# Optimization experiments

Measured on AMD Instinct MI355X. Metric: run time of the kernel, lower is better.

The kernel has to match this reference:

```python
import jax, jax.numpy as jnp
import numpy as np

B, T, C = 2, 4096, 768
H = 12
D = C // H  # head_dim = 64

def setup_inputs() -> dict:
    key = jax.random.key(0)
    ks = jax.random.split(key, 5)
    s = 1.0 / np.sqrt(C)
    return {
        "x": jax.random.normal(ks[0], (B, T, C), dtype=jnp.float32),
        "qkv_w": jax.random.normal(ks[1], (C, 3 * C), dtype=jnp.float32) * s,
        "qkv_b": jax.random.normal(ks[2], (3 * C,), dtype=jnp.float32) * 0.02,
        "out_w": jax.random.normal(ks[3], (C, C), dtype=jnp.float32) * s,
        "out_b": jax.random.normal(ks[4], (C,), dtype=jnp.float32) * 0.02,
    }

def reference(x, qkv_w, qkv_b, out_w, out_b):
    b, t, c = x.shape
    qkv = x @ qkv_w + qkv_b                      # [B,T,3C]
    q, k, v = jnp.split(qkv, 3, axis=-1)
    # [B,T,C] -> [B,H,T,D]
    q = q.reshape(b, t, H, D).transpose(0, 2, 1, 3)
    k = k.reshape(b, t, H, D).transpose(0, 2, 1, 3)
    v = v.reshape(b, t, H, D).transpose(0, 2, 1, 3)
    scale = 1.0 / np.sqrt(D)
    attn = jnp.einsum('bhqd,bhkd->bhqk', q, k) * scale  # [B,H,T,T]
    causal = jnp.tril(jnp.ones((t, t), dtype=bool))
    attn = jnp.where(causal, attn, -jnp.inf)
    attn = jax.nn.softmax(attn, axis=-1)
    y = jnp.einsum('bhqk,bhkd->bhqd', attn, v)           # [B,H,T,D]
    y = y.transpose(0, 2, 1, 3).reshape(b, t, c)
    return y @ out_w + out_b
```

## Files before the change

### kernel.cpp

```cpp
#include <hip/hip_runtime.h>
#include <hip/hip_bf16.h>

#define T_SEQ 4096
#define C_DIM 768
#define H_NUM 12
#define D_HEAD 64
#define N3    2304
#define BHN   24

typedef __bf16 bf16x8 __attribute__((ext_vector_type(8)));
typedef float  f32x4  __attribute__((ext_vector_type(4)));

__device__ inline unsigned short f2b(float f) {
    unsigned int x = __float_as_uint(f);
    unsigned int r = (x + 0x7FFFu + ((x >> 16) & 1u)) >> 16;
    return (unsigned short)r;
}

__device__ inline unsigned int pack_trunc(float lo, float hi) {
    return __builtin_amdgcn_perm(__float_as_uint(hi), __float_as_uint(lo), 0x07060302u);
}

__device__ inline void load_lds16(const unsigned short* g, unsigned short* l) {
    __builtin_amdgcn_global_load_lds(
        (const __attribute__((address_space(1))) unsigned int*)(g),
        (__attribute__((address_space(3))) unsigned int*)(l),
        16, 0, 0);
}

__global__ __launch_bounds__(256) void convert_bf16(
    const float* __restrict__ in, unsigned short* __restrict__ out, int n4)
{
    int idx = blockIdx.x * 256 + threadIdx.x;
    if (idx < n4) {
        float4 v = reinterpret_cast<const float4*>(in)[idx];
        ushort4 u;
        u.x = f2b(v.x); u.y = f2b(v.y); u.z = f2b(v.z); u.w = f2b(v.w);
        reinterpret_cast<ushort4*>(out)[idx] = u;
    }
}

__global__ __launch_bounds__(256) void transpose_bf16(
    const float* __restrict__ in, unsigned short* __restrict__ out, int R, int Cc)
{
    __shared__ unsigned short Ts[64 * 72];
    const int k0 = blockIdx.x * 64, n0 = blockIdx.y * 64;
    const int tid = threadIdx.x;
    #pragma unroll
    for (int it = 0; it < 4; ++it) {
        int idx = tid + it * 256;
        int r = idx >> 4, c4 = idx & 15;
        float4 v = *reinterpret_cast<const float4*>(&in[(size_t)(k0 + r) * Cc + n0 + c4 * 4]);
        Ts[(c4 * 4 + 0) * 72 + r] = f2b(v.x);
        Ts[(c4 * 4 + 1) * 72 + r] = f2b(v.y);
        Ts[(c4 * 4 + 2) * 72 + r] = f2b(v.z);
        Ts[(c4 * 4 + 3) * 72 + r] = f2b(v.w);
    }
    __syncthreads();
    #pragma unroll
    for (int it = 0; it < 2; ++it) {
        int idx = tid + it * 256;
        int row = idx >> 3, ch = idx & 7;
        *reinterpret_cast<uint4*>(&out[(size_t)(n0 + row) * R + k0 + ch * 8]) =
            *reinterpret_cast<const uint4*>(&Ts[row * 72 + ch * 8]);
    }
}

__global__ __launch_bounds__(256) void qkv_gemm(
    const unsigned short* __restrict__ xb, const unsigned short* __restrict__ wt,
    const float* __restrict__ bias,
    unsigned short* __restrict__ Q, unsigned short* __restrict__ K,
    unsigned short* __restrict__ Vt)
{
    __shared__ unsigned short SH[128 * 128];
    unsigned short* As = SH;
    unsigned short* Bs = SH + 128 * 64;
    const int tid  = threadIdx.x;
    const int m0   = blockIdx.x * 128;
    const int n0   = blockIdx.y * 128;
    const int lane = tid & 63;
    const int wv   = tid >> 6;
    const int wr   = wv >> 1, wc = wv & 1;
    const int quad = lane >> 4;
    const int lr   = lane & 15;
    const int srow = lane >> 3;
    const int dch  = (lane & 7) ^ srow;

    f32x4 acc[4][4] = {};

    for (int kk = 0; kk < C_DIM; kk += 64) {
        __syncthreads();
        #pragma unroll
        for (int i = 0; i < 4; ++i) {
            int inst = wv * 4 + i;
            int r = inst * 8 + srow;
            load_lds16(xb + (size_t)(m0 + r) * C_DIM + kk + dch * 8, As + inst * 512);
            load_lds16(wt + (size_t)(n0 + r) * C_DIM + kk + dch * 8, Bs + inst * 512);
        }
        __syncthreads();
        #pragma unroll
        for (int k2 = 0; k2 < 2; ++k2) {
            bf16x8 af[4], bf[4];
            #pragma unroll
            for (int mt = 0; mt < 4; ++mt)
                af[mt] = *reinterpret_cast<const bf16x8*>(
                    &As[(wr * 64 + mt * 16 + lr) * 64 + (((k2 * 4 + quad) ^ (lr & 7)) * 8)]);
            #pragma unroll
            for (int nt = 0; nt < 4; ++nt)
                bf[nt] = *reinterpret_cast<const bf16x8*>(
                    &Bs[(wc * 64 + nt * 16 + lr) * 64 + (((k2 * 4 + quad) ^ (lr & 7)) * 8)]);
            #pragma unroll
            for (int mt = 0; mt < 4; ++mt)
                #pragma unroll
                for (int nt = 0; nt < 4; ++nt)
                    acc[mt][nt] = __builtin_amdgcn_mfma_f32_16x16x32_bf16(af[mt], bf[nt], acc[mt][nt], 0, 0, 0);
        }
    }

    const int whichblk = n0 / C_DIM;
    if (whichblk == 2) {
        __syncthreads();
        #pragma unroll
        for (int nt = 0; nt < 4; ++nt) {
            int dp = wc * 64 + nt * 16 + lr;
            float bj = bias[n0 + dp];
            #pragma unroll
            for (int mt = 0; mt < 4; ++mt) {
                int t0 = wr * 64 + mt * 16 + quad * 4;
                ushort4 u;
                u.x = f2b(acc[mt][nt][0] + bj);
                u.y = f2b(acc[mt][nt][1] + bj);
                u.z = f2b(acc[mt][nt][2] + bj);
                u.w = f2b(acc[mt][nt][3] + bj);
                int cs = (t0 >> 2) ^ ((dp & 15) << 1);
                *reinterpret_cast<ushort4*>(&SH[dp * 128 + cs * 4]) = u;
            }
        }
        __syncthreads();
        const int bb = m0 >> 12;
        const int t_base = m0 & 4095;
        const int h_base = (n0 - 2 * C_DIM) >> 6;
        #pragma unroll
        for (int i = 0; i < 8; ++i) {
            int idx = i * 256 + tid;
            int row = idx >> 4, cc = idx & 15;
            int pc = ((2 * cc) ^ ((row & 15) << 1)) * 4;
            uint4 val = *reinterpret_cast<const uint4*>(&SH[row * 128 + pc]);
            int head = h_base + (row >> 6);
            int d = row & 63;
            *reinterpret_cast<uint4*>(
                &Vt[((size_t)(bb * H_NUM + head) * D_HEAD + d) * T_SEQ + t_base + cc * 8]) = val;
        }
    } else {
        const int head0 = ((n0 % C_DIM) + wc * 64) >> 6;
        #pragma unroll
        for (int nt = 0; nt < 4; ++nt) {
            int d = nt * 16 + lr;
            float bj = bias[n0 + wc * 64 + nt * 16 + lr];
            #pragma unroll
            for (int mt = 0; mt < 4; ++mt) {
                #pragma unroll
                for (int reg = 0; reg < 4; ++reg) {
                    int i = m0 + wr * 64 + mt * 16 + quad * 4 + reg;
                    int bb = i >> 12, t = i & 4095;
                    float val = acc[mt][nt][reg] + bj;
                    size_t base = (size_t)(bb * H_NUM + head0) * T_SEQ + t;
                    if (whichblk == 0)
                        Q[base * D_HEAD + d] = f2b(val * 0.18033688011f);
                    else
                        K[base * D_HEAD + d] = f2b(val);
                }
            }
        }
    }
}

__global__ __launch_bounds__(256, 4) void flash_attn(
    const unsigned short* __restrict__ Q, const unsigned short* __restrict__ K,
    const unsigned short* __restrict__ Vt, unsigned short* __restrict__ Y)
{
    __shared__ unsigned short Ks[64 * 64];
    __shared__ unsigned short Vs[64 * 64];
    __shared__ unsigned short Ps[64 * 72];
    const int tid  = threadIdx.x;
    const int lane = tid & 63;
    const int wv   = tid >> 6;
    const int quad = lane >> 4;
    const int lr   = lane & 15;
    const int srow = lane >> 3;
    const int dch  = (lane & 7) ^ srow;

    const int bid = blockIdx.x;
    const int qt  = 63 - (bid / BHN);
    const int bh  = bid % BHN;
    const int q0  = qt * 64;

    const unsigned short* Qb = Q  + (size_t)bh * T_SEQ * D_HEAD;
    const unsigned short* Kb = K  + (size_t)bh * T_SEQ * D_HEAD;
    const unsigned short* Vb = Vt + (size_t)bh * D_HEAD * T_SEQ;

    const int qg = q0 + wv * 16 + lr;
    bf16x8 bQ[2];
    #pragma unroll
    for (int k2 = 0; k2 < 2; ++k2)
        bQ[k2] = *reinterpret_cast<const bf16x8*>(
            &Qb[(size_t)qg * D_HEAD + k2 * 32 + quad * 8]);

    f32x4 oacc[4] = {};
    float l_ = 0.f;

    for (int kt = 0; kt <= qt; ++kt) {
        __syncthreads();
        #pragma unroll
        for (int i = 0; i < 2; ++i) {
            int inst = wv * 2 + i;
            int r = inst * 8 + srow;
            load_lds16(Kb + (size_t)(kt * 64 + r) * D_HEAD + dch * 8, Ks + inst * 512);
            load_lds16(Vb + (size_t)r * T_SEQ + kt * 64 + dch * 8, Vs + inst * 512);
        }
        __syncthreads();

        f32x4 st[4];
        #pragma unroll
        for (int mt = 0; mt < 4; ++mt) {
            bf16x8 aK0 = *reinterpret_cast<const bf16x8*>(
                &Ks[(mt * 16 + lr) * 64 + ((quad ^ (lr & 7)) * 8)]);
            bf16x8 aK1 = *reinterpret_cast<const bf16x8*>(
                &Ks[(mt * 16 + lr) * 64 + (((4 + quad) ^ (lr & 7)) * 8)]);
            f32x4 a = {};
            a = __builtin_amdgcn_mfma_f32_16x16x32_bf16(aK0, bQ[0], a, 0, 0, 0);
            a = __builtin_amdgcn_mfma_f32_16x16x32_bf16(aK1, bQ[1], a, 0, 0, 0);
            st[mt] = a;
        }

        if (kt == qt) {
            #pragma unroll
            for (int mt = 0; mt < 4; ++mt)
                #pragma unroll
                for (int reg = 0; reg < 4; ++reg)
                    if (kt * 64 + mt * 16 + quad * 4 + reg > qg) st[mt][reg] = -INFINITY;
        }

        #pragma unroll
        for (int mt = 0; mt < 4; ++mt)
            #pragma unroll
            for (int reg = 0; reg < 4; ++reg) {
                float p = exp2f(st[mt][reg]);
                st[mt][reg] = p;
                l_ += p;
            }

        #pragma unroll
        for (int mt = 0; mt < 4; ++mt) {
            uint2 u;
            u.x = pack_trunc(st[mt][0], st[mt][1]);
            u.y = pack_trunc(st[mt][2], st[mt][3]);
            *reinterpret_cast<uint2*>(&Ps[(wv * 16 + lr) * 72 + mt * 16 + quad * 4]) = u;
        }

        bf16x8 bP0 = *reinterpret_cast<const bf16x8*>(&Ps[(wv * 16 + lr) * 72 + quad * 8]);
        bf16x8 bP1 = *reinterpret_cast<const bf16x8*>(&Ps[(wv * 16 + lr) * 72 + 32 + quad * 8]);
        #pragma unroll
        for (int dt = 0; dt < 4; ++dt) {
            bf16x8 aV0 = *reinterpret_cast<const bf16x8*>(
                &Vs[(dt * 16 + lr) * 64 + ((quad ^ (lr & 7)) * 8)]);
            bf16x8 aV1 = *reinterpret_cast<const bf16x8*>(
                &Vs[(dt * 16 + lr) * 64 + (((4 + quad) ^ (lr & 7)) * 8)]);
            oacc[dt] = __builtin_amdgcn_mfma_f32_16x16x32_bf16(aV0, bP0, oacc[dt], 0, 0, 0);
            oacc[dt] = __builtin_amdgcn_mfma_f32_16x16x32_bf16(aV1, bP1, oacc[dt], 0, 0, 0);
        }
    }

    l_ += __shfl_xor(l_, 16);
    l_ += __shfl_xor(l_, 32);
    float inv = 1.f / l_;
    const int bb = bh / H_NUM, hh = bh % H_NUM;
    #pragma unroll
    for (int dt = 0; dt < 4; ++dt) {
        ushort4 u;
        u.x = f2b(oacc[dt][0] * inv);
        u.y = f2b(oacc[dt][1] * inv);
        u.z = f2b(oacc[dt][2] * inv);
        u.w = f2b(oacc[dt][3] * inv);
        *reinterpret_cast<ushort4*>(
            &Y[(size_t)(bb * T_SEQ + qg) * C_DIM + hh * 64 + dt * 16 + quad * 4]) = u;
    }
}

__global__ __launch_bounds__(256) void out_gemm(
    const unsigned short* __restrict__ Y, const unsigned short* __restrict__ wt,
    const float* __restrict__ bias, float* __restrict__ out)
{
    __shared__ unsigned short As[128 * 64];
    __shared__ unsigned short Bs[64 * 64];
    const int tid  = threadIdx.x;
    const int m0   = blockIdx.x * 128;
    const int n0   = blockIdx.y * 64;
    const int lane = tid & 63;
    const int wv   = tid >> 6;
    const int wr   = wv >> 1, wc = wv & 1;
    const int quad = lane >> 4;
    const int lr   = lane & 15;
    const int srow = lane >> 3;
    const int dch  = (lane & 7) ^ srow;

    f32x4 acc[4][2] = {};

    for (int kk = 0; kk < C_DIM; kk += 64) {
        __syncthreads();
        #pragma unroll
        for (int i = 0; i < 4; ++i) {
            int inst = wv * 4 + i;
            int r = inst * 8 + srow;
            load_lds16(Y + (size_t)(m0 + r) * C_DIM + kk + dch * 8, As + inst * 512);
        }
        #pragma unroll
        for (int i = 0; i < 2; ++i) {
            int inst = wv * 2 + i;
            int r = inst * 8 + srow;
            load_lds16(wt + (size_t)(n0 + r) * C_DIM + kk + dch * 8, Bs + inst * 512);
        }
        __syncthreads();
        #pragma unroll
        for (int k2 = 0; k2 < 2; ++k2) {
            bf16x8 af[4], bf[2];
            #pragma unroll
            for (int mt = 0; mt < 4; ++mt)
                af[mt] = *reinterpret_cast<const bf16x8*>(
                    &As[(wr * 64 + mt * 16 + lr) * 64 + (((k2 * 4 + quad) ^ (lr & 7)) * 8)]);
            #pragma unroll
            for (int nt = 0; nt < 2; ++nt)
                bf[nt] = *reinterpret_cast<const bf16x8*>(
                    &Bs[(wc * 32 + nt * 16 + lr) * 64 + (((k2 * 4 + quad) ^ (lr & 7)) * 8)]);
            #pragma unroll
            for (int mt = 0; mt < 4; ++mt)
                #pragma unroll
                for (int nt = 0; nt < 2; ++nt)
                    acc[mt][nt] = __builtin_amdgcn_mfma_f32_16x16x32_bf16(af[mt], bf[nt], acc[mt][nt], 0, 0, 0);
        }
    }

    #pragma unroll
    for (int nt = 0; nt < 2; ++nt) {
        int j = n0 + wc * 32 + nt * 16 + lr;
        float bj = bias[j];
        #pragma unroll
        for (int mt = 0; mt < 4; ++mt)
            #pragma unroll
            for (int reg = 0; reg < 4; ++reg) {
                int i = m0 + wr * 64 + mt * 16 + quad * 4 + reg;
                out[(size_t)i * C_DIM + j] = acc[mt][nt][reg] + bj;
            }
    }
}

extern "C" void kernel_launch(void* const* d_in, const int* in_sizes, int n_in,
                              void* d_out, int out_size, void* d_ws, size_t ws_size,
                              hipStream_t stream) {
    const float* x     = (const float*)d_in[0];
    const float* qkv_w = (const float*)d_in[1];
    const float* qkv_b = (const float*)d_in[2];
    const float* out_w = (const float*)d_in[3];
    const float* out_b = (const float*)d_in[4];
    float* out = (float*)d_out;

    unsigned short* xb  = (unsigned short*)d_ws;
    unsigned short* wtq = xb  + (size_t)8192 * 768;
    unsigned short* wto = wtq + (size_t)2304 * 768;
    unsigned short* Qs  = wto + (size_t)768 * 768;
    unsigned short* Kg  = Qs  + (size_t)BHN * T_SEQ * D_HEAD;
    unsigned short* Vt  = Kg  + (size_t)BHN * T_SEQ * D_HEAD;
    unsigned short* Y   = xb;

    convert_bf16 <<<6144, 256, 0, stream>>>(x, xb, (8192 * 768) / 4);
    transpose_bf16<<<dim3(12, 36), 256, 0, stream>>>(qkv_w, wtq, C_DIM, N3);
    transpose_bf16<<<dim3(12, 12), 256, 0, stream>>>(out_w, wto, C_DIM, C_DIM);
    qkv_gemm  <<<dim3(64, 18), 256, 0, stream>>>(xb, wtq, qkv_b, Qs, Kg, Vt);
    flash_attn<<<dim3(64 * BHN), 256, 0, stream>>>(Qs, Kg, Vt, Y);
    out_gemm  <<<dim3(64, 12), 256, 0, stream>>>(Y, wto, out_b, out);
}
```

Baseline: 250.4 us.

## Split key tiles across waves in flash attention with LDS reduction epilogue

Each wave now owns all 64 queries of the block and handles every fourth key tile, loading K and V fragments directly from global memory into registers. This replaces the shared K/V LDS staging and the two block barriers per tile. The row sums are computed with an MFMA against a ones vector, and partial outputs are reduced across waves through LDS at the end. In exchange, register pressure rises (occupancy bound lowered to 2), global loads are no longer shared across waves, and small diagonal blocks leave some waves idle.

```diff
diff --git a/kernel.cpp b/kernel.cpp
--- a/kernel.cpp
+++ b/kernel.cpp
@@ -175,20 +175,19 @@
     }
 }
 
-__global__ __launch_bounds__(256, 4) void flash_attn(
+__global__ __launch_bounds__(256, 2) void flash_attn(
     const unsigned short* __restrict__ Q, const unsigned short* __restrict__ K,
     const unsigned short* __restrict__ Vt, unsigned short* __restrict__ Y)
 {
-    __shared__ unsigned short Ks[64 * 64];
-    __shared__ unsigned short Vs[64 * 64];
-    __shared__ unsigned short Ps[64 * 72];
+    __shared__ union {
+        unsigned short Ps[4][16 * 72];
+        struct { float Of[64][68]; float ls[4][64]; } ep;
+    } sh;
     const int tid  = threadIdx.x;
     const int lane = tid & 63;
     const int wv   = tid >> 6;
     const int quad = lane >> 4;
     const int lr   = lane & 15;
-    const int srow = lane >> 3;
-    const int dch  = (lane & 7) ^ srow;
 
     const int bid = blockIdx.x;
     const int qt  = 63 - (bid / BHN);
@@ -199,91 +198,119 @@
     const unsigned short* Kb = K  + (size_t)bh * T_SEQ * D_HEAD;
     const unsigned short* Vb = Vt + (size_t)bh * D_HEAD * T_SEQ;
 
-    const int qg = q0 + wv * 16 + lr;
-    bf16x8 bQ[2];
-    #pragma unroll
-    for (int k2 = 0; k2 < 2; ++k2)
-        bQ[k2] = *reinterpret_cast<const bf16x8*>(
-            &Qb[(size_t)qg * D_HEAD + k2 * 32 + quad * 8]);
-
-    f32x4 oacc[4] = {};
-    float l_ = 0.f;
-
-    for (int kt = 0; kt <= qt; ++kt) {
-        __syncthreads();
-        #pragma unroll
-        for (int i = 0; i < 2; ++i) {
-            int inst = wv * 2 + i;
-            int r = inst * 8 + srow;
-            load_lds16(Kb + (size_t)(kt * 64 + r) * D_HEAD + dch * 8, Ks + inst * 512);
-            load_lds16(Vb + (size_t)r * T_SEQ + kt * 64 + dch * 8, Vs + inst * 512);
-        }
-        __syncthreads();
-
-        f32x4 st[4];
-        #pragma unroll
-        for (int mt = 0; mt < 4; ++mt) {
-            bf16x8 aK0 = *reinterpret_cast<const bf16x8*>(
-                &Ks[(mt * 16 + lr) * 64 + ((quad ^ (lr & 7)) * 8)]);
-            bf16x8 aK1 = *reinterpret_cast<const bf16x8*>(
-                &Ks[(mt * 16 + lr) * 64 + (((4 + quad) ^ (lr & 7)) * 8)]);
-            f32x4 a = {};
-            a = __builtin_amdgcn_mfma_f32_16x16x32_bf16(aK0, bQ[0], a, 0, 0, 0);
-            a = __builtin_amdgcn_mfma_f32_16x16x32_bf16(aK1, bQ[1], a, 0, 0, 0);
-            st[mt] = a;
-        }
-
-        if (kt == qt) {
+    bf16x8 bQ[4][2];
+    #pragma unroll
+    for (int qg = 0; qg < 4; ++qg)
+        #pragma unroll
+        for (int k2 = 0; k2 < 2; ++k2)
+            bQ[qg][k2] = *reinterpret_cast<const bf16x8*>(
+                &Qb[(size_t)(q0 + qg * 16 + lr) * D_HEAD + k2 * 32 + quad * 8]);
+
+    bf16x8 ones;
+    #pragma unroll
+    for (int i = 0; i < 8; ++i) ones[i] = (__bf16)1.0f;
+
+    f32x4 oacc[4][4] = {};
+    f32x4 lacc[4] = {};
+
+    unsigned short* Pw = sh.Ps[wv];
+
+    for (int kt = wv; kt <= qt; kt += 4) {
+        const unsigned short* Kt = Kb + (size_t)kt * 64 * D_HEAD;
+        bf16x8 aK[4][2], aV[4][2];
+        #pragma unroll
+        for (int mt = 0; mt < 4; ++mt)
+            #pragma unroll
+            for (int k2 = 0; k2 < 2; ++k2) {
+                aK[mt][k2] = *reinterpret_cast<const bf16x8*>(
+                    &Kt[(mt * 16 + lr) * D_HEAD + k2 * 32 + quad * 8]);
+                aV[mt][k2] = *reinterpret_cast<const bf16x8*>(
+                    &Vb[(size_t)(mt * 16 + lr) * T_SEQ + kt * 64 + k2 * 32 + quad * 8]);
+            }
+        const bool isdiag = (kt == qt);
+
+        #pragma unroll
+        for (int qg = 0; qg < 4; ++qg) {
+            f32x4 st[4];
+            #pragma unroll
+            for (int mt = 0; mt < 4; ++mt) {
+                f32x4 a = {};
+                a = __builtin_amdgcn_mfma_f32_16x16x32_bf16(aK[mt][0], bQ[qg][0], a, 0, 0, 0);
+                a = __builtin_amdgcn_mfma_f32_16x16x32_bf16(aK[mt][1], bQ[qg][1], a, 0, 0, 0);
+                st[mt] = a;
+            }
+            if (isdiag) {
+                int qq = qg * 16 + lr;
+                #pragma unroll
+                for (int mt = 0; mt < 4; ++mt)
+                    #pragma unroll
+                    for (int reg = 0; reg < 4; ++reg)
+                        if (mt * 16 + quad * 4 + reg > qq) st[mt][reg] = -INFINITY;
+            }
             #pragma unroll
             for (int mt = 0; mt < 4; ++mt)
                 #pragma unroll
                 for (int reg = 0; reg < 4; ++reg)
-                    if (kt * 64 + mt * 16 + quad * 4 + reg > qg) st[mt][reg] = -INFINITY;
-        }
-
-        #pragma unroll
-        for (int mt = 0; mt < 4; ++mt)
-            #pragma unroll
-            for (int reg = 0; reg < 4; ++reg) {
-                float p = exp2f(st[mt][reg]);
-                st[mt][reg] = p;
-                l_ += p;
-            }
-
-        #pragma unroll
-        for (int mt = 0; mt < 4; ++mt) {
-            uint2 u;
-            u.x = pack_trunc(st[mt][0], st[mt][1]);
-            u.y = pack_trunc(st[mt][2], st[mt][3]);
-            *reinterpret_cast<uint2*>(&Ps[(wv * 16 + lr) * 72 + mt * 16 + quad * 4]) = u;
-        }
-
-        bf16x8 bP0 = *reinterpret_cast<const bf16x8*>(&Ps[(wv * 16 + lr) * 72 + quad * 8]);
-        bf16x8 bP1 = *reinterpret_cast<const bf16x8*>(&Ps[(wv * 16 + lr) * 72 + 32 + quad * 8]);
-        #pragma unroll
-        for (int dt = 0; dt < 4; ++dt) {
-            bf16x8 aV0 = *reinterpret_cast<const bf16x8*>(
-                &Vs[(dt * 16 + lr) * 64 + ((quad ^ (lr & 7)) * 8)]);
-            bf16x8 aV1 = *reinterpret_cast<const bf16x8*>(
-                &Vs[(dt * 16 + lr) * 64 + (((4 + quad) ^ (lr & 7)) * 8)]);
-            oacc[dt] = __builtin_amdgcn_mfma_f32_16x16x32_bf16(aV0, bP0, oacc[dt], 0, 0, 0);
-            oacc[dt] = __builtin_amdgcn_mfma_f32_16x16x32_bf16(aV1, bP1, oacc[dt], 0, 0, 0);
-        }
-    }
-
-    l_ += __shfl_xor(l_, 16);
-    l_ += __shfl_xor(l_, 32);
-    float inv = 1.f / l_;
+                    st[mt][reg] = exp2f(st[mt][reg]);
+
+            #pragma unroll
+            for (int mt = 0; mt < 4; ++mt) {
+                uint2 u;
+                u.x = pack_trunc(st[mt][0], st[mt][1]);
+                u.y = pack_trunc(st[mt][2], st[mt][3]);
+                *reinterpret_cast<uint2*>(&Pw[lr * 72 + mt * 16 + quad * 4]) = u;
+            }
+            bf16x8 bP0 = *reinterpret_cast<const bf16x8*>(&Pw[lr * 72 + quad * 8]);
+            bf16x8 bP1 = *reinterpret_cast<const bf16x8*>(&Pw[lr * 72 + 32 + quad * 8]);
+
+            #pragma unroll
+            for (int dt = 0; dt < 4; ++dt) {
+                oacc[qg][dt] = __builtin_amdgcn_mfma_f32_16x16x32_bf16(aV[dt][0], bP0, oacc[qg][dt], 0, 0, 0);
+                oacc[qg][dt] = __builtin_amdgcn_mfma_f32_16x16x32_bf16(aV[dt][1], bP1, oacc[qg][dt], 0, 0, 0);
+            }
+            lacc[qg] = __builtin_amdgcn_mfma_f32_16x16x32_bf16(ones, bP0, lacc[qg], 0, 0, 0);
+            lacc[qg] = __builtin_amdgcn_mfma_f32_16x16x32_bf16(ones, bP1, lacc[qg], 0, 0, 0);
+        }
+    }
+
+    __syncthreads();
+    if (quad == 0) {
+        #pragma unroll
+        for (int qg = 0; qg < 4; ++qg)
+            sh.ep.ls[wv][qg * 16 + lr] = lacc[qg][0];
+    }
+    #pragma unroll
+    for (int p = 0; p < 4; ++p) {
+        int dq = (wv + p) & 3;
+        #pragma unroll
+        for (int qg = 0; qg < 4; ++qg) {
+            float* dst = &sh.ep.Of[qg * 16 + lr][dq * 16 + quad * 4];
+            f32x4 v = oacc[qg][dq];
+            if (p) v += *reinterpret_cast<const f32x4*>(dst);
+            *reinterpret_cast<f32x4*>(dst) = v;
+        }
+        __syncthreads();
+    }
+
     const int bb = bh / H_NUM, hh = bh % H_NUM;
-    #pragma unroll
-    for (int dt = 0; dt < 4; ++dt) {
-        ushort4 u;
-        u.x = f2b(oacc[dt][0] * inv);
-        u.y = f2b(oacc[dt][1] * inv);
-        u.z = f2b(oacc[dt][2] * inv);
-        u.w = f2b(oacc[dt][3] * inv);
-        *reinterpret_cast<ushort4*>(
-            &Y[(size_t)(bb * T_SEQ + qg) * C_DIM + hh * 64 + dt * 16 + quad * 4]) = u;
+    {
+        int q  = tid >> 2;
+        int ds = (tid & 3) * 16;
+        float lt = sh.ep.ls[0][q] + sh.ep.ls[1][q] + sh.ep.ls[2][q] + sh.ep.ls[3][q];
+        float inv = 1.f / lt;
+        float o[16];
+        #pragma unroll
+        for (int i = 0; i < 4; ++i) {
+            f32x4 t = *reinterpret_cast<const f32x4*>(&sh.ep.Of[q][ds + i * 4]);
+            o[i * 4 + 0] = t[0]; o[i * 4 + 1] = t[1]; o[i * 4 + 2] = t[2]; o[i * 4 + 3] = t[3];
+        }
+        unsigned int u[8];
+        #pragma unroll
+        for (int i = 0; i < 8; ++i)
+            u[i] = (unsigned int)f2b(o[2 * i] * inv) | ((unsigned int)f2b(o[2 * i + 1] * inv) << 16);
+        unsigned short* yp = &Y[(size_t)(bb * T_SEQ + q0 + q) * C_DIM + hh * 64 + ds];
+        *reinterpret_cast<uint4*>(yp)     = make_uint4(u[0], u[1], u[2], u[3]);
+        *reinterpret_cast<uint4*>(yp + 8) = make_uint4(u[4], u[5], u[6], u[7]);
     }
 }
 
```

New measurement: 287.3 us. 1.15x slower.

## Process two query tiles per attention block and merge prep kernels into one launch

Applied to the files above, without the earlier changes.

The flash attention kernel now handles 128 query rows per block as two 64-row halves. Each K/V tile loaded into LDS is reused for both halves, which halves K/V global traffic and the number of block barriers. The K and V fragments are held in registers, and the occupancy hint drops from 4 to 3 blocks per CU to make room for them. Separately, the bf16 conversion of x and the two weight transposes are fused into a single prep launch to save launch overhead, at the cost of fewer attention blocks and coarser load balancing.

```diff
diff --git a/kernel.cpp b/kernel.cpp
--- a/kernel.cpp
+++ b/kernel.cpp
@@ -28,24 +28,11 @@
         16, 0, 0);
 }
 
-__global__ __launch_bounds__(256) void convert_bf16(
-    const float* __restrict__ in, unsigned short* __restrict__ out, int n4)
+__device__ inline void transpose_tile(const float* __restrict__ in,
+                                      unsigned short* __restrict__ out,
+                                      unsigned short* Ts, int k0, int n0,
+                                      int R, int Cc, int tid)
 {
-    int idx = blockIdx.x * 256 + threadIdx.x;
-    if (idx < n4) {
-        float4 v = reinterpret_cast<const float4*>(in)[idx];
-        ushort4 u;
-        u.x = f2b(v.x); u.y = f2b(v.y); u.z = f2b(v.z); u.w = f2b(v.w);
-        reinterpret_cast<ushort4*>(out)[idx] = u;
-    }
-}
-
-__global__ __launch_bounds__(256) void transpose_bf16(
-    const float* __restrict__ in, unsigned short* __restrict__ out, int R, int Cc)
-{
-    __shared__ unsigned short Ts[64 * 72];
-    const int k0 = blockIdx.x * 64, n0 = blockIdx.y * 64;
-    const int tid = threadIdx.x;
     #pragma unroll
     for (int it = 0; it < 4; ++it) {
         int idx = tid + it * 256;
@@ -63,6 +50,29 @@
         int row = idx >> 3, ch = idx & 7;
         *reinterpret_cast<uint4*>(&out[(size_t)(n0 + row) * R + k0 + ch * 8]) =
             *reinterpret_cast<const uint4*>(&Ts[row * 72 + ch * 8]);
+    }
+}
+
+__global__ __launch_bounds__(256) void prep(
+    const float* __restrict__ x, const float* __restrict__ qkv_w,
+    const float* __restrict__ out_w,
+    unsigned short* __restrict__ xb, unsigned short* __restrict__ wtq,
+    unsigned short* __restrict__ wto)
+{
+    __shared__ unsigned short Ts[64 * 72];
+    const int b = blockIdx.x, tid = threadIdx.x;
+    if (b < 6144) {
+        int idx = b * 256 + tid;
+        float4 v = reinterpret_cast<const float4*>(x)[idx];
+        ushort4 u;
+        u.x = f2b(v.x); u.y = f2b(v.y); u.z = f2b(v.z); u.w = f2b(v.w);
+        reinterpret_cast<ushort4*>(xb)[idx] = u;
+    } else if (b < 6576) {
+        int bb = b - 6144;
+        transpose_tile(qkv_w, wtq, Ts, (bb % 12) * 64, (bb / 12) * 64, C_DIM, N3, tid);
+    } else {
+        int bb = b - 6576;
+        transpose_tile(out_w, wto, Ts, (bb % 12) * 64, (bb / 12) * 64, C_DIM, C_DIM, tid);
     }
 }
 
@@ -175,7 +185,7 @@
     }
 }
 
-__global__ __launch_bounds__(256, 4) void flash_attn(
+__global__ __launch_bounds__(256, 3) void flash_attn(
     const unsigned short* __restrict__ Q, const unsigned short* __restrict__ K,
     const unsigned short* __restrict__ Vt, unsigned short* __restrict__ Y)
 {
@@ -191,25 +201,29 @@
     const int dch  = (lane & 7) ^ srow;
 
     const int bid = blockIdx.x;
-    const int qt  = 63 - (bid / BHN);
+    const int qt  = 31 - (bid / BHN);
     const int bh  = bid % BHN;
-    const int q0  = qt * 64;
+    const int q0  = qt * 128;
+    const int diag0 = 2 * qt;
 
     const unsigned short* Qb = Q  + (size_t)bh * T_SEQ * D_HEAD;
     const unsigned short* Kb = K  + (size_t)bh * T_SEQ * D_HEAD;
     const unsigned short* Vb = Vt + (size_t)bh * D_HEAD * T_SEQ;
 
-    const int qg = q0 + wv * 16 + lr;
-    bf16x8 bQ[2];
+    bf16x8 bQ[2][2];
     #pragma unroll
-    for (int k2 = 0; k2 < 2; ++k2)
-        bQ[k2] = *reinterpret_cast<const bf16x8*>(
-            &Qb[(size_t)qg * D_HEAD + k2 * 32 + quad * 8]);
-
-    f32x4 oacc[4] = {};
-    float l_ = 0.f;
-
-    for (int kt = 0; kt <= qt; ++kt) {
+    for (int h = 0; h < 2; ++h)
+        #pragma unroll
+        for (int k2 = 0; k2 < 2; ++k2)
+            bQ[h][k2] = *reinterpret_cast<const bf16x8*>(
+                &Qb[(size_t)(q0 + h * 64 + wv * 16 + lr) * D_HEAD + k2 * 32 + quad * 8]);
+
+    f32x4 oacc[2][4] = {};
+    float l_[2] = {0.f, 0.f};
+
+    unsigned short* Pw = &Ps[(wv * 16) * 72];
+
+    for (int kt = 0; kt <= diag0 + 1; ++kt) {
         __syncthreads();
         #pragma unroll
         for (int i = 0; i < 2; ++i) {
@@ -220,70 +234,79 @@
         }
         __syncthreads();
 
-        f32x4 st[4];
-        #pragma unroll
-        for (int mt = 0; mt < 4; ++mt) {
-            bf16x8 aK0 = *reinterpret_cast<const bf16x8*>(
-                &Ks[(mt * 16 + lr) * 64 + ((quad ^ (lr & 7)) * 8)]);
-            bf16x8 aK1 = *reinterpret_cast<const bf16x8*>(
-                &Ks[(mt * 16 + lr) * 64 + (((4 + quad) ^ (lr & 7)) * 8)]);
-            f32x4 a = {};
-            a = __builtin_amdgcn_mfma_f32_16x16x32_bf16(aK0, bQ[0], a, 0, 0, 0);
-            a = __builtin_amdgcn_mfma_f32_16x16x32_bf16(aK1, bQ[1], a, 0, 0, 0);
-            st[mt] = a;
-        }
-
-        if (kt == qt) {
+        bf16x8 aK[4][2], aV[4][2];
+        #pragma unroll
+        for (int mt = 0; mt < 4; ++mt)
+            #pragma unroll
+            for (int k2 = 0; k2 < 2; ++k2) {
+                aK[mt][k2] = *reinterpret_cast<const bf16x8*>(
+                    &Ks[(mt * 16 + lr) * 64 + (((k2 * 4 + quad) ^ (lr & 7)) * 8)]);
+                aV[mt][k2] = *reinterpret_cast<const bf16x8*>(
+                    &Vs[(mt * 16 + lr) * 64 + (((k2 * 4 + quad) ^ (lr & 7)) * 8)]);
+            }
+
+        #pragma unroll
+        for (int h = 0; h < 2; ++h) {
+            if (h == 0 && kt > diag0) continue;
+            f32x4 st[4];
+            #pragma unroll
+            for (int mt = 0; mt < 4; ++mt) {
+                f32x4 a = {};
+                a = __builtin_amdgcn_mfma_f32_16x16x32_bf16(aK[mt][0], bQ[h][0], a, 0, 0, 0);
+                a = __builtin_amdgcn_mfma_f32_16x16x32_bf16(aK[mt][1], bQ[h][1], a, 0, 0, 0);
+                st[mt] = a;
+            }
+            const int qg = q0 + h * 64 + wv * 16 + lr;
+            if (kt == diag0 + h) {
+                #pragma unroll
+                for (int mt = 0; mt < 4; ++mt)
+                    #pragma unroll
+                    for (int reg = 0; reg < 4; ++reg)
+                        if (kt * 64 + mt * 16 + quad * 4 + reg > qg) st[mt][reg] = -INFINITY;
+            }
             #pragma unroll
             for (int mt = 0; mt < 4; ++mt)
                 #pragma unroll
-                for (int reg = 0; reg < 4; ++reg)
-                    if (kt * 64 + mt * 16 + quad * 4 + reg > qg) st[mt][reg] = -INFINITY;
-        }
-
-        #pragma unroll
-        for (int mt = 0; mt < 4; ++mt)
-            #pragma unroll
-            for (int reg = 0; reg < 4; ++reg) {
-                float p = exp2f(st[mt][reg]);
-                st[mt][reg] = p;
-                l_ += p;
-            }
-
-        #pragma unroll
-        for (int mt = 0; mt < 4; ++mt) {
-            uint2 u;
-            u.x = pack_trunc(st[mt][0], st[mt][1]);
-            u.y = pack_trunc(st[mt][2], st[mt][3]);
-            *reinterpret_cast<uint2*>(&Ps[(wv * 16 + lr) * 72 + mt * 16 + quad * 4]) = u;
-        }
-
-        bf16x8 bP0 = *reinterpret_cast<const bf16x8*>(&Ps[(wv * 16 + lr) * 72 + quad * 8]);
-        bf16x8 bP1 = *reinterpret_cast<const bf16x8*>(&Ps[(wv * 16 + lr) * 72 + 32 + quad * 8]);
-        #pragma unroll
-        for (int dt = 0; dt < 4; ++dt) {
-            bf16x8 aV0 = *reinterpret_cast<const bf16x8*>(
-                &Vs[(dt * 16 + lr) * 64 + ((quad ^ (lr & 7)) * 8)]);
-            bf16x8 aV1 = *reinterpret_cast<const bf16x8*>(
-                &Vs[(dt * 16 + lr) * 64 + (((4 + quad) ^ (lr & 7)) * 8)]);
-            oacc[dt] = __builtin_amdgcn_mfma_f32_16x16x32_bf16(aV0, bP0, oacc[dt], 0, 0, 0);
-            oacc[dt] = __builtin_amdgcn_mfma_f32_16x16x32_bf16(aV1, bP1, oacc[dt], 0, 0, 0);
-        }
-    }
-
-    l_ += __shfl_xor(l_, 16);
-    l_ += __shfl_xor(l_, 32);
-    float inv = 1.f / l_;
+                for (int reg = 0; reg < 4; ++reg) {
+                    float p = exp2f(st[mt][reg]);
+                    st[mt][reg] = p;
+                    l_[h] += p;
+                }
+            #pragma unroll
+            for (int mt = 0; mt < 4; ++mt) {
+                uint2 u;
+                u.x = pack_trunc(st[mt][0], st[mt][1]);
+                u.y = pack_trunc(st[mt][2], st[mt][3]);
+                *reinterpret_cast<uint2*>(&Pw[lr * 72 + mt * 16 + quad * 4]) = u;
+            }
+            bf16x8 bP0 = *reinterpret_cast<const bf16x8*>(&Pw[lr * 72 + quad * 8]);
+            bf16x8 bP1 = *reinterpret_cast<const bf16x8*>(&Pw[lr * 72 + 32 + quad * 8]);
+            #pragma unroll
+            for (int dt = 0; dt < 4; ++dt) {
+                oacc[h][dt] = __builtin_amdgcn_mfma_f32_16x16x32_bf16(aV[dt][0], bP0, oacc[h][dt], 0, 0, 0);
+                oacc[h][dt] = __builtin_amdgcn_mfma_f32_16x16x32_bf16(aV[dt][1], bP1, oacc[h][dt], 0, 0, 0);
+            }
+        }
+    }
+
     const int bb = bh / H_NUM, hh = bh % H_NUM;
     #pragma unroll
-    for (int dt = 0; dt < 4; ++dt) {
-        ushort4 u;
-        u.x = f2b(oacc[dt][0] * inv);
-        u.y = f2b(oacc[dt][1] * inv);
-        u.z = f2b(oacc[dt][2] * inv);
-        u.w = f2b(oacc[dt][3] * inv);
-        *reinterpret_cast<ushort4*>(
-            &Y[(size_t)(bb * T_SEQ + qg) * C_DIM + hh * 64 + dt * 16 + quad * 4]) = u;
+    for (int h = 0; h < 2; ++h) {
+        float lt = l_[h];
+        lt += __shfl_xor(lt, 16);
+        lt += __shfl_xor(lt, 32);
+        float inv = 1.f / lt;
+        int q = q0 + h * 64 + wv * 16 + lr;
+        #pragma unroll
+        for (int dt = 0; dt < 4; ++dt) {
+            ushort4 u;
+            u.x = f2b(oacc[h][dt][0] * inv);
+            u.y = f2b(oacc[h][dt][1] * inv);
+            u.z = f2b(oacc[h][dt][2] * inv);
+            u.w = f2b(oacc[h][dt][3] * inv);
+            *reinterpret_cast<ushort4*>(
+                &Y[(size_t)(bb * T_SEQ + q) * C_DIM + hh * 64 + dt * 16 + quad * 4]) = u;
+        }
     }
 }
 
@@ -372,10 +395,8 @@
     unsigned short* Vt  = Kg  + (size_t)BHN * T_SEQ * D_HEAD;
     unsigned short* Y   = xb;
 
-    convert_bf16 <<<6144, 256, 0, stream>>>(x, xb, (8192 * 768) / 4);
-    transpose_bf16<<<dim3(12, 36), 256, 0, stream>>>(qkv_w, wtq, C_DIM, N3);
-    transpose_bf16<<<dim3(12, 12), 256, 0, stream>>>(out_w, wto, C_DIM, C_DIM);
+    prep      <<<6720, 256, 0, stream>>>(x, qkv_w, out_w, xb, wtq, wto);
     qkv_gemm  <<<dim3(64, 18), 256, 0, stream>>>(xb, wtq, qkv_b, Qs, Kg, Vt);
-    flash_attn<<<dim3(64 * BHN), 256, 0, stream>>>(Qs, Kg, Vt, Y);
+    flash_attn<<<dim3(32 * BHN), 256, 0, stream>>>(Qs, Kg, Vt, Y);
     out_gemm  <<<dim3(64, 12), 256, 0, stream>>>(Y, wto, out_b, out);
 }
```

Result: no change. 248.7 us (-0.7%).
